# Performance work log

Hardware: AMD Instinct MI355X
Metric: run time of the kernel (lower is better)

## Reference

```python
import jax, jax.numpy as jnp
import numpy as np

T, B, IN, H, OUT = 2048, 512, 27, 64, 26
EPS = 1e-5
DROP = 0.1


def setup_inputs() -> dict:
    key = jax.random.key(0)
    ks = jax.random.split(key, 11)
    s = 1.0 / np.sqrt(H)
    u = lambda k, shape: jax.random.uniform(k, shape, jnp.float32, -s, s)
    return {
        "obscure_word": jax.random.normal(ks[0], (T, B, IN), jnp.float32),
        "prev_guess": jax.random.uniform(ks[1], (T, OUT), jnp.float32),
        "W_ih": u(ks[2], (4 * H, IN)),
        "W_hh": u(ks[3], (4 * H, H)),
        "b_ih": u(ks[4], (4 * H,)),
        "b_hh": u(ks[5], (4 * H,)),
        "gamma": jnp.ones((H,), jnp.float32),
        "beta": jnp.zeros((H,), jnp.float32),
        "W_fc": u(ks[6], (OUT, H + OUT)),
        "b_fc": u(ks[7], (OUT,)),
        # LockedDropout mask: sampled once, reused every timestep, pre-scaled by 1/(1-p)
        "drop_mask": (jax.random.uniform(ks[8], (B, H)) < (1.0 - DROP)).astype(jnp.float32) / (1.0 - DROP),
    }


def reference(obscure_word, prev_guess, W_ih, W_hh, b_ih, b_hh, gamma, beta, W_fc, b_fc, drop_mask):
    h0 = jnp.zeros((B, H), obscure_word.dtype)
    c0 = jnp.zeros((B, H), obscure_word.dtype)

    def step(carry, inputs):
        h, c = carry
        x_t, pg_t = inputs  # [B, IN], [OUT]
        gates = x_t @ W_ih.T + b_ih + h @ W_hh.T + b_hh  # [B, 4H]
        i, f, g, o = jnp.split(gates, 4, axis=1)
        i = jax.nn.sigmoid(i)
        f = jax.nn.sigmoid(f)
        g = jnp.tanh(g)
        o = jax.nn.sigmoid(o)
        c_new = f * c + i * g
        h_new = o * jnp.tanh(c_new)
        # BatchNorm1d (training mode: per-timestep batch stats, biased var)
        mean = jnp.mean(h_new, axis=0)
        var = jnp.mean((h_new - mean) ** 2, axis=0)
        hb = (h_new - mean) * jax.lax.rsqrt(var + EPS) * gamma + beta
        # LockedDropout (same mask every timestep)
        hd = hb * drop_mask
        # MaxPool1d over batch dim -> [H]
        pooled = jnp.max(hd, axis=0)
        out = jnp.concatenate([pooled, pg_t])  # [H+OUT]
        y = out @ W_fc.T + b_fc  # [OUT]
        return (h_new, c_new), y

    _, ys = jax.lax.scan(step, (h0, c0), (obscure_word, prev_guess))
    return ys[:, None, :]  # [T, 1, OUT]
```

## Files before the change

### kernel.cpp

```cpp
#include <hip/hip_runtime.h>
#include <hip/hip_bf16.h>

#define TT   2048
#define BB   512
#define IN_  27
#define HH   64
#define NG   256
#define OUTD 26
#define EPSV 1e-5f
#define RT   64

__device__ __forceinline__ float sigm(float x) {
    return 1.0f / (1.0f + __expf(-x));
}

__device__ __forceinline__ float tanh_fast(float x) {
    float e = __expf(-2.0f * fabsf(x));
    float r = (1.0f - e) / (1.0f + e);
    return copysignf(r, x);
}

#define PIN16(a,b,c,d,e,f,g,h,i,jj,k,ll,m,n,o,p) \
    asm volatile("" : "+v"(a),"+v"(b),"+v"(c),"+v"(d),"+v"(e),"+v"(f),"+v"(g),"+v"(h), \
                      "+v"(i),"+v"(jj),"+v"(k),"+v"(ll),"+v"(m),"+v"(n),"+v"(o),"+v"(p));

__global__ __launch_bounds__(256, 4) void gate_x_pre(
    const float* __restrict__ x,
    const float* __restrict__ W_ih,
    const float* __restrict__ b_ih,
    const float* __restrict__ b_hh,
    float* __restrict__ gate_x,
    int row0, int nrows)
{
    const int j = threadIdx.x;
    __shared__ float w_s[NG * 28];
    __shared__ float x_s[RT * 28];

#pragma unroll
    for (int s = 0; s < 27; ++s) {
        const int idx = j + s * 256;
        const int r = idx / 27;
        const int c = idx - r * 27;
        w_s[r * 28 + c] = W_ih[idx];
    }
    const int rbase = blockIdx.x * RT;
    const float* xsrc = x + (size_t)(row0 + rbase) * IN_;
#pragma unroll
    for (int s = 0; s < 7; ++s) {
        const int idx = j + s * 256;
        if (idx < RT * IN_) {
            const int r = idx / 27;
            const int c = idx - r * 27;
            x_s[r * 28 + c] = xsrc[idx];
        }
    }
    __syncthreads();

    const float4* wr4 = (const float4*)(w_s + j * 28);
    float4 q0 = wr4[0], q1 = wr4[1], q2 = wr4[2], q3 = wr4[3];
    float4 q4 = wr4[4], q5 = wr4[5], q6 = wr4[6];
    const float bias = b_ih[j] + b_hh[j];

    float* out = gate_x + (size_t)rbase * NG + j;
#pragma unroll 4
    for (int r = 0; r < RT; ++r) {
        const float4* xr4 = (const float4*)(x_s + r * 28);
        const float4 p0 = xr4[0], p1 = xr4[1], p2 = xr4[2], p3 = xr4[3];
        const float4 p4 = xr4[4], p5 = xr4[5], p6 = xr4[6];
        float a0 = bias, a1 = 0.0f, a2 = 0.0f, a3 = 0.0f;
        a0 = fmaf(q0.x, p0.x, a0); a1 = fmaf(q0.y, p0.y, a1);
        a2 = fmaf(q0.z, p0.z, a2); a3 = fmaf(q0.w, p0.w, a3);
        a0 = fmaf(q1.x, p1.x, a0); a1 = fmaf(q1.y, p1.y, a1);
        a2 = fmaf(q1.z, p1.z, a2); a3 = fmaf(q1.w, p1.w, a3);
        a0 = fmaf(q2.x, p2.x, a0); a1 = fmaf(q2.y, p2.y, a1);
        a2 = fmaf(q2.z, p2.z, a2); a3 = fmaf(q2.w, p2.w, a3);
        a0 = fmaf(q3.x, p3.x, a0); a1 = fmaf(q3.y, p3.y, a1);
        a2 = fmaf(q3.z, p3.z, a2); a3 = fmaf(q3.w, p3.w, a3);
        a0 = fmaf(q4.x, p4.x, a0); a1 = fmaf(q4.y, p4.y, a1);
        a2 = fmaf(q4.z, p4.z, a2); a3 = fmaf(q4.w, p4.w, a3);
        a0 = fmaf(q5.x, p5.x, a0); a1 = fmaf(q5.y, p5.y, a1);
        a2 = fmaf(q5.z, p5.z, a2); a3 = fmaf(q5.w, p5.w, a3);
        a0 = fmaf(q6.x, p6.x, a0); a1 = fmaf(q6.y, p6.y, a1);
        a2 = fmaf(q6.z, p6.z, a2);
        out[(size_t)r * NG] = (a0 + a1) + (a2 + a3);
    }
}

__global__ __launch_bounds__(256, 2) void lstm_seq(
    const float* __restrict__ gate_x,
    const float* __restrict__ W_hh,
    float* __restrict__ h_all,
    float* __restrict__ state,
    int tc, int first)
{
    const int b = blockIdx.x;
    const int j = threadIdx.x;
    const int q = j >> 6;
    const int l = j & 63;

    const float4* whv = (const float4*)W_hh + (size_t)j * 16;
    float4 v0 = whv[0],  v1 = whv[1],  v2 = whv[2],  v3 = whv[3];
    float4 v4 = whv[4],  v5 = whv[5],  v6 = whv[6],  v7 = whv[7];
    float4 v8 = whv[8],  v9 = whv[9],  v10 = whv[10], v11 = whv[11];
    float4 v12 = whv[12], v13 = whv[13], v14 = whv[14], v15 = whv[15];
#define UNP(m, V) float wh##m##0=(V).x, wh##m##1=(V).y, wh##m##2=(V).z, wh##m##3=(V).w;
    UNP(0,v0) UNP(1,v1) UNP(2,v2) UNP(3,v3) UNP(4,v4) UNP(5,v5) UNP(6,v6) UNP(7,v7)
    UNP(8,v8) UNP(9,v9) UNP(10,v10) UNP(11,v11) UNP(12,v12) UNP(13,v13) UNP(14,v14) UNP(15,v15)
#undef UNP
    PIN16(wh00,wh01,wh02,wh03, wh10,wh11,wh12,wh13, wh20,wh21,wh22,wh23, wh30,wh31,wh32,wh33)
    PIN16(wh40,wh41,wh42,wh43, wh50,wh51,wh52,wh53, wh60,wh61,wh62,wh63, wh70,wh71,wh72,wh73)
    PIN16(wh80,wh81,wh82,wh83, wh90,wh91,wh92,wh93, wh100,wh101,wh102,wh103, wh110,wh111,wh112,wh113)
    PIN16(wh120,wh121,wh122,wh123, wh130,wh131,wh132,wh133, wh140,wh141,wh142,wh143, wh150,wh151,wh152,wh153)

    float cv, hcur;
    if (first) { cv = 0.0f; hcur = 0.0f; }
    else {
        hcur = state[b * HH + l];
        cv   = state[BB * HH + b * HH + l];
    }

    __shared__ float  acts[NG];
    __shared__ float4 hbuf[16];

    if (q == 0) ((float*)hbuf)[l] = hcur;
    __syncthreads();

    const size_t stride = (size_t)BB * NG;
    const float* gbase = gate_x + (size_t)b * NG + j;

    float gx0 = gbase[0];
    float gx1 = (tc > 1) ? gbase[stride] : gx0;

    for (int tl = 0; tl < tc; ++tl) {
        const int t2 = (tl + 2 < tc) ? (tl + 2) : (tc - 1);
        const float gx2 = gbase[(size_t)t2 * stride];

        float a0 = gx0, a1 = 0.0f, a2 = 0.0f, a3 = 0.0f;
#define HD(m) { float4 h4 = hbuf[m]; \
        a0 = fmaf(h4.x, wh##m##0, a0); \
        a1 = fmaf(h4.y, wh##m##1, a1); \
        a2 = fmaf(h4.z, wh##m##2, a2); \
        a3 = fmaf(h4.w, wh##m##3, a3); }
        HD(0) HD(1) HD(2) HD(3) HD(4) HD(5) HD(6) HD(7)
        HD(8) HD(9) HD(10) HD(11) HD(12) HD(13) HD(14) HD(15)
#undef HD
        const float acc = (a0 + a1) + (a2 + a3);

        const float av = (q == 2) ? tanh_fast(acc) : sigm(acc);
        acts[j] = av;
        __syncthreads();

        const float gi = acts[l];
        const float gf = acts[HH + l];
        const float gg = acts[2 * HH + l];
        const float go = acts[3 * HH + l];

        const float cn = fmaf(gf, cv, gi * gg);
        const float hn = go * tanh_fast(cn);
        cv = cn;
        hcur = hn;

        if (q == 0) {
            ((float*)hbuf)[l] = hn;
            h_all[((size_t)tl * BB + b) * HH + l] = hn;
        }
        __syncthreads();
        gx0 = gx1;
        gx1 = gx2;
    }

    if (q == 0) {
        state[b * HH + l] = hcur;
        state[BB * HH + b * HH + l] = cv;
    }
}

__global__ __launch_bounds__(256, 2) void bn_pool_fc(
    const float* __restrict__ h_all,
    const float* __restrict__ gamma,
    const float* __restrict__ beta,
    const float* __restrict__ dmask,
    const float* __restrict__ pg,
    const float* __restrict__ W_fc,
    const float* __restrict__ b_fc,
    float* __restrict__ y,
    int t0, int tc)
{
    const int tl = blockIdx.x;
    const int t = t0 + tl;
    const int tid = threadIdx.x;
    const int g = tid >> 6;
    const int hcol = tid & 63;
    const float* hp = h_all + (size_t)tl * BB * HH;

    __shared__ float s_a[4][HH];
    __shared__ float s_b[4][HH];
    __shared__ float s_scale[HH];
    __shared__ float s_shift[HH];
    __shared__ float s_pool[HH];

    float sum = 0.0f, sq = 0.0f;
    for (int bb = g; bb < BB; bb += 4) {
        const float v = hp[bb * HH + hcol];
        sum += v;
        sq = fmaf(v, v, sq);
    }
    s_a[g][hcol] = sum;
    s_b[g][hcol] = sq;
    __syncthreads();

    if (tid < HH) {
        const float s  = (s_a[0][tid] + s_a[1][tid]) + (s_a[2][tid] + s_a[3][tid]);
        const float q2 = (s_b[0][tid] + s_b[1][tid]) + (s_b[2][tid] + s_b[3][tid]);
        const float mean = s * (1.0f / BB);
        const float var  = q2 * (1.0f / BB) - mean * mean;
        const float rs = rsqrtf(var + EPSV);
        const float sc = rs * gamma[tid];
        s_scale[tid] = sc;
        s_shift[tid] = beta[tid] - mean * sc;
    }
    __syncthreads();

    const float sc = s_scale[hcol];
    const float sh = s_shift[hcol];
    float m = -3.0e38f;
    for (int bb = g; bb < BB; bb += 4) {
        const float v = hp[bb * HH + hcol];
        const float hd = fmaf(v, sc, sh) * dmask[bb * HH + hcol];
        m = fmaxf(m, hd);
    }
    s_a[g][hcol] = m;
    __syncthreads();
    if (tid < HH) {
        s_pool[tid] = fmaxf(fmaxf(s_a[0][tid], s_a[1][tid]),
                            fmaxf(s_a[2][tid], s_a[3][tid]));
    }
    __syncthreads();

    if (tid < OUTD) {
        float acc = b_fc[tid];
        const float* w = W_fc + tid * (HH + OUTD);
#pragma unroll
        for (int k = 0; k < HH; ++k) acc = fmaf(w[k], s_pool[k], acc);
#pragma unroll
        for (int k = 0; k < OUTD; ++k) acc = fmaf(w[HH + k], pg[t * OUTD + k], acc);
        y[t * OUTD + tid] = acc;
    }
}

extern "C" void kernel_launch(void* const* d_in, const int* in_sizes, int n_in,
                              void* d_out, int out_size, void* d_ws, size_t ws_size,
                              hipStream_t stream)
{
    const float* x     = (const float*)d_in[0];
    const float* pg    = (const float*)d_in[1];
    const float* W_ih  = (const float*)d_in[2];
    const float* W_hh  = (const float*)d_in[3];
    const float* b_ih  = (const float*)d_in[4];
    const float* b_hh  = (const float*)d_in[5];
    const float* gamma = (const float*)d_in[6];
    const float* beta  = (const float*)d_in[7];
    const float* W_fc  = (const float*)d_in[8];
    const float* b_fc  = (const float*)d_in[9];
    const float* dmask = (const float*)d_in[10];
    float* y = (float*)d_out;

    const size_t state_bytes = 2ull * BB * HH * sizeof(float);
    const size_t per_t = (size_t)BB * HH * sizeof(float) + (size_t)BB * NG * sizeof(float);
    size_t avail = (ws_size > state_bytes) ? (ws_size - state_bytes) : 0;
    int chunkT = (int)(avail / per_t);
    if (chunkT > TT) chunkT = TT;
    if (chunkT < 1) chunkT = 1;

    float* h_all  = (float*)d_ws;
    float* gate_x = h_all + (size_t)chunkT * BB * HH;
    float* state  = gate_x + (size_t)chunkT * BB * NG;

    int first = 1;
    for (int t0 = 0; t0 < TT; t0 += chunkT) {
        int tc = TT - t0;
        if (tc > chunkT) tc = chunkT;
        const int nrows = tc * BB;
        gate_x_pre<<<nrows / RT, 256, 0, stream>>>(x, W_ih, b_ih, b_hh,
                                                   gate_x, t0 * BB, nrows);
        lstm_seq<<<BB, 256, 0, stream>>>(gate_x, W_hh, h_all, state, tc, first);
        bn_pool_fc<<<tc, 256, 0, stream>>>(h_all, gamma, beta, dmask, pg,
                                           W_fc, b_fc, y, t0, tc);
        first = 0;
    }
}
```

Baseline: 2.366 ms.

## Broadcast hidden state via readlane and double-buffer gate activations to drop a barrier

Every wave already computes the full new hidden vector redundantly, so each thread now keeps its own h element in a register. The h·W_hh product reads the other 63 elements with readlane instead of going through a shared-memory h buffer. The activations buffer is double-buffered by timestep parity, which allows removing the second __syncthreads per step. The cost is 64 scalar readlane ops per step in place of 16 vector LDS reads, plus a launch-attribute change to waves_per_eu(2,2).

```diff
diff --git a/kernel.cpp b/kernel.cpp
--- a/kernel.cpp
+++ b/kernel.cpp
@@ -23,6 +23,8 @@
 #define PIN16(a,b,c,d,e,f,g,h,i,jj,k,ll,m,n,o,p) \
     asm volatile("" : "+v"(a),"+v"(b),"+v"(c),"+v"(d),"+v"(e),"+v"(f),"+v"(g),"+v"(h), \
                       "+v"(i),"+v"(jj),"+v"(k),"+v"(ll),"+v"(m),"+v"(n),"+v"(o),"+v"(p));
+
+#define RLH(k) __int_as_float(__builtin_amdgcn_readlane(__float_as_int(hv), (k)))
 
 __global__ __launch_bounds__(256, 4) void gate_x_pre(
     const float* __restrict__ x,
@@ -86,7 +88,9 @@
     }
 }
 
-__global__ __launch_bounds__(256, 2) void lstm_seq(
+__global__ __attribute__((amdgpu_flat_work_group_size(256, 256)))
+           __attribute__((amdgpu_waves_per_eu(2, 2)))
+void lstm_seq(
     const float* __restrict__ gate_x,
     const float* __restrict__ W_hh,
     float* __restrict__ h_all,
@@ -112,18 +116,14 @@
     PIN16(wh80,wh81,wh82,wh83, wh90,wh91,wh92,wh93, wh100,wh101,wh102,wh103, wh110,wh111,wh112,wh113)
     PIN16(wh120,wh121,wh122,wh123, wh130,wh131,wh132,wh133, wh140,wh141,wh142,wh143, wh150,wh151,wh152,wh153)
 
-    float cv, hcur;
-    if (first) { cv = 0.0f; hcur = 0.0f; }
+    float cv, hv;
+    if (first) { cv = 0.0f; hv = 0.0f; }
     else {
-        hcur = state[b * HH + l];
-        cv   = state[BB * HH + b * HH + l];
-    }
-
-    __shared__ float  acts[NG];
-    __shared__ float4 hbuf[16];
-
-    if (q == 0) ((float*)hbuf)[l] = hcur;
-    __syncthreads();
+        hv = state[b * HH + l];
+        cv = state[BB * HH + b * HH + l];
+    }
+
+    __shared__ float acts[2][NG];
 
     const size_t stride = (size_t)BB * NG;
     const float* gbase = gate_x + (size_t)b * NG + j;
@@ -136,41 +136,38 @@
         const float gx2 = gbase[(size_t)t2 * stride];
 
         float a0 = gx0, a1 = 0.0f, a2 = 0.0f, a3 = 0.0f;
-#define HD(m) { float4 h4 = hbuf[m]; \
-        a0 = fmaf(h4.x, wh##m##0, a0); \
-        a1 = fmaf(h4.y, wh##m##1, a1); \
-        a2 = fmaf(h4.z, wh##m##2, a2); \
-        a3 = fmaf(h4.w, wh##m##3, a3); }
+#define HD(m) \
+        a0 = fmaf(RLH(4*(m)+0), wh##m##0, a0); \
+        a1 = fmaf(RLH(4*(m)+1), wh##m##1, a1); \
+        a2 = fmaf(RLH(4*(m)+2), wh##m##2, a2); \
+        a3 = fmaf(RLH(4*(m)+3), wh##m##3, a3);
         HD(0) HD(1) HD(2) HD(3) HD(4) HD(5) HD(6) HD(7)
         HD(8) HD(9) HD(10) HD(11) HD(12) HD(13) HD(14) HD(15)
 #undef HD
         const float acc = (a0 + a1) + (a2 + a3);
 
         const float av = (q == 2) ? tanh_fast(acc) : sigm(acc);
-        acts[j] = av;
+        acts[tl & 1][j] = av;
         __syncthreads();
 
-        const float gi = acts[l];
-        const float gf = acts[HH + l];
-        const float gg = acts[2 * HH + l];
-        const float go = acts[3 * HH + l];
+        const float gi = acts[tl & 1][l];
+        const float gf = acts[tl & 1][HH + l];
+        const float gg = acts[tl & 1][2 * HH + l];
+        const float go = acts[tl & 1][3 * HH + l];
 
         const float cn = fmaf(gf, cv, gi * gg);
         const float hn = go * tanh_fast(cn);
         cv = cn;
-        hcur = hn;
-
-        if (q == 0) {
-            ((float*)hbuf)[l] = hn;
-            h_all[((size_t)tl * BB + b) * HH + l] = hn;
-        }
-        __syncthreads();
+        hv = hn;
+
+        if (q == 0) h_all[((size_t)tl * BB + b) * HH + l] = hn;
+
         gx0 = gx1;
         gx1 = gx2;
     }
 
     if (q == 0) {
-        state[b * HH + l] = hcur;
+        state[b * HH + l] = hv;
         state[BB * HH + b * HH + l] = cv;
     }
 }
```

New measurement: 2.432 ms. 2.8% more time.
